# Kernel tuning notes

Measured on AMD Instinct MI355X. Metric: run time of the kernel, lower is better.

Reference implementation:

```python
import jax, jax.numpy as jnp
import numpy as np

FRAME_LENGTH = 2048
HOP_LENGTH = 512


def setup_inputs() -> dict:
    key = jax.random.key(0)
    # (batch, num_channels, samples): 8 clips, stereo, 30 s @ 16 kHz
    x = jax.random.normal(key, (8, 2, 480000), dtype=jnp.float32)
    return {"x": x}


def reference(x):
    """Faithful Enframe.forward.

    The original applies a Conv1d whose weight is the identity matrix
    torch.eye(FL)[:, None, :] with stride=hop, per channel, then concatenates
    channel results along dim=1. Mathematically out[b, n*FL + k, t] =
    x[b, n, t*hop + k]. We implement it as a strided gather (the efficient
    form of the same math).
    """
    B, C, S = x.shape
    FL, HOP = FRAME_LENGTH, HOP_LENGTH
    T = (S - FL) // HOP + 1  # frames_num = 934 for S=480000
    # gather_idx[k, t] = t*HOP + k  -> (FL, T)
    gather_idx = jnp.arange(FL)[:, None] + jnp.arange(T)[None, :] * HOP
    frames = x[:, :, gather_idx]  # (B, C, FL, T)
    # torch.cat over channel dim puts channel-major blocks of size FL on dim 1
    return frames.reshape(B, C * FL, T)
```

## Files before the change

kernel.cpp:

```cpp
#include <hip/hip_runtime.h>


constexpr int FL  = 2048;
constexpr int HOP = 512;
constexpr int TT  = 64;
constexpr int RT  = 64;
constexpr int ROWS = TT + 3;
constexpr int LSTR = RT + 1;

__global__ __launch_bounds__(256)
void enframe_kernel(const float* __restrict__ x, float* __restrict__ out,
                    int S, int T) {
    __shared__ float lds[ROWS * LSTR];

    const int bc = blockIdx.x;
    const int t0 = blockIdx.y * TT;
    const int r0 = blockIdx.z * RT;
    const int tid = threadIdx.x;

    {
        const int rg   = tid & 15;
        const int row0 = tid >> 4;
        const float* xb = x + (size_t)bc * S;
#pragma unroll
        for (int p = 0; p < 5; ++p) {
            const int row = p * 16 + row0;
            if (row < ROWS) {
                const size_t base = (size_t)(t0 + row) * HOP + r0;
                if (base + RT <= (size_t)S) {
                    const float4 v = *(const float4*)(xb + base + rg * 4);
                    float* l = lds + row * LSTR + rg * 4;
                    l[0] = v.x; l[1] = v.y; l[2] = v.z; l[3] = v.w;
                }
            }
        }
    }
    __syncthreads();

    const int tg = tid & 15;
    const int ko = tid >> 4;
    const int tl = tg * 4;
    const int t  = t0 + tl;
    float* ob = out + (size_t)bc * FL * T;
    const bool full = (t + 3 < T);
#pragma unroll
    for (int rb = 0; rb < RT; rb += 16) {
        const int rr = rb + ko;
        const int kb = r0 + rr;
#pragma unroll
        for (int h = 0; h < 4; ++h) {
            const int k = h * HOP + kb;
            const float* l = lds + (tl + h) * LSTR + rr;
            if (full) {
                float4 v = { l[0 * LSTR], l[1 * LSTR], l[2 * LSTR], l[3 * LSTR] };
                *(float4*)(ob + (size_t)k * T + t) = v;
            } else {
#pragma unroll
                for (int j = 0; j < 4; ++j)
                    if (t + j < T) ob[(size_t)k * T + t + j] = l[j * LSTR];
            }
        }
    }
}

extern "C" void kernel_launch(void* const* d_in, const int* in_sizes, int n_in,
                              void* d_out, int out_size, void* d_ws, size_t ws_size,
                              hipStream_t stream) {
    const float* x = (const float*)d_in[0];
    float* out = (float*)d_out;
    const int BC = 16;
    const int S  = in_sizes[0] / BC;
    const int T  = (S - FL) / HOP + 1;
    const int t_tiles = (T + TT - 1) / TT;
    const int r_tiles = HOP / RT;
    dim3 grid(BC, (unsigned)t_tiles, (unsigned)r_tiles);
    enframe_kernel<<<grid, 256, 0, stream>>>(x, out, S, T);
}
```

Baseline: 151.1 us.

## Retile enframe so each block writes a contiguous output slab with nontemporal stores

Each block now handles one (batch-channel, hop-offset h, 16-row k group) and stages a full 16×T transposed tile in LDS. The output region for those 16 consecutive k rows is contiguous, so stores become flat coalesced float4 writes, issued as nontemporal stores. This is meant to cut strided partial-line writes and per-tile overheads, at the cost of 1024-thread blocks, large LDS use that limits occupancy, bank conflicts on the transposed LDS writes, and a hardcoded TMAX that assumes T ≤ 934.

```diff
diff --git a/kernel.cpp b/kernel.cpp
--- a/kernel.cpp
+++ b/kernel.cpp
@@ -1,63 +1,54 @@
 #include <hip/hip_runtime.h>
 
 
-constexpr int FL  = 2048;
-constexpr int HOP = 512;
-constexpr int TT  = 64;
-constexpr int RT  = 64;
-constexpr int ROWS = TT + 3;
-constexpr int LSTR = RT + 1;
+constexpr int FL   = 2048;
+constexpr int HOP  = 512;
+constexpr int KT   = 16;
+constexpr int TMAX = 934;
+constexpr int NTHR = 1024;
 
-__global__ __launch_bounds__(256)
+typedef float vf4 __attribute__((ext_vector_type(4)));
+
+__global__ __launch_bounds__(NTHR)
 void enframe_kernel(const float* __restrict__ x, float* __restrict__ out,
                     int S, int T) {
-    __shared__ float lds[ROWS * LSTR];
+    __shared__ float lds[KT * TMAX];
 
     const int bc = blockIdx.x;
-    const int t0 = blockIdx.y * TT;
-    const int r0 = blockIdx.z * RT;
+    const int h  = blockIdx.y;
+    const int r0 = blockIdx.z * KT;
     const int tid = threadIdx.x;
 
+    const float* xb = x + (size_t)bc * S;
+    float* ob = out + ((size_t)bc * FL + (size_t)h * HOP + r0) * (size_t)T;
+
     {
-        const int rg   = tid & 15;
-        const int row0 = tid >> 4;
-        const float* xb = x + (size_t)bc * S;
+        const int c4 = tid & 3;
+        const int trow = tid >> 2;
 #pragma unroll
-        for (int p = 0; p < 5; ++p) {
-            const int row = p * 16 + row0;
-            if (row < ROWS) {
-                const size_t base = (size_t)(t0 + row) * HOP + r0;
-                if (base + RT <= (size_t)S) {
-                    const float4 v = *(const float4*)(xb + base + rg * 4);
-                    float* l = lds + row * LSTR + rg * 4;
-                    l[0] = v.x; l[1] = v.y; l[2] = v.z; l[3] = v.w;
+        for (int it = 0; it < 4; ++it) {
+            const int t = it * (NTHR / 4) + trow;
+            if (t < T) {
+                const size_t g = (size_t)(t + h) * HOP + r0 + c4 * 4;
+                if (g + 4 <= (size_t)S) {
+                    const vf4 v = *(const vf4*)(xb + g);
+                    float* l = lds + (size_t)(c4 * 4) * T + t;
+                    l[0 * T] = v.x; l[1 * T] = v.y;
+                    l[2 * T] = v.z; l[3 * T] = v.w;
                 }
             }
         }
     }
     __syncthreads();
 
-    const int tg = tid & 15;
-    const int ko = tid >> 4;
-    const int tl = tg * 4;
-    const int t  = t0 + tl;
-    float* ob = out + (size_t)bc * FL * T;
-    const bool full = (t + 3 < T);
+    {
+        const int nq = KT * T / 4;
 #pragma unroll
-    for (int rb = 0; rb < RT; rb += 16) {
-        const int rr = rb + ko;
-        const int kb = r0 + rr;
-#pragma unroll
-        for (int h = 0; h < 4; ++h) {
-            const int k = h * HOP + kb;
-            const float* l = lds + (tl + h) * LSTR + rr;
-            if (full) {
-                float4 v = { l[0 * LSTR], l[1 * LSTR], l[2 * LSTR], l[3 * LSTR] };
-                *(float4*)(ob + (size_t)k * T + t) = v;
-            } else {
-#pragma unroll
-                for (int j = 0; j < 4; ++j)
-                    if (t + j < T) ob[(size_t)k * T + t + j] = l[j * LSTR];
+        for (int it = 0; it < 4; ++it) {
+            const int q = it * NTHR + tid;
+            if (q < nq) {
+                const vf4 v = *(const vf4*)(lds + (size_t)q * 4);
+                __builtin_nontemporal_store(v, (vf4*)(ob + (size_t)q * 4));
             }
         }
     }
@@ -71,8 +62,7 @@
     const int BC = 16;
     const int S  = in_sizes[0] / BC;
     const int T  = (S - FL) / HOP + 1;
-    const int t_tiles = (T + TT - 1) / TT;
-    const int r_tiles = HOP / RT;
-    dim3 grid(BC, (unsigned)t_tiles, (unsigned)r_tiles);
-    enframe_kernel<<<grid, 256, 0, stream>>>(x, out, S, T);
+    const int r_tiles = HOP / KT;
+    dim3 grid(BC, 4u, (unsigned)r_tiles);
+    enframe_kernel<<<grid, NTHR, 0, stream>>>(x, out, S, T);
 }
```

After: 161.5 us. +6.9%, slower.
